# Optimization experiments

Hardware: AMD Instinct MI355X
Metric: run time of the kernel (lower is better)

Reference implementation:

```python
import jax, jax.numpy as jnp
import numpy as np

N_ITERATIONS = 3
N_OUT_CAPS = 10


def squash(t, axis=-2):
    # squash(s) = ||s||^2 * s / ((1 + ||s||^2) * ||s||)
    sqr_norm = jnp.sum(t * t, axis=axis, keepdims=True)
    norm = jnp.sqrt(sqr_norm)
    return sqr_norm * t / ((1.0 + sqr_norm) * norm)


def setup_inputs() -> dict:
    key = jax.random.key(0)
    B, I, O, D = 256, 1152, 10, 16
    u_hat = jax.random.normal(key, (B, I, O, D, 1), dtype=jnp.float32)
    return {"u_hat": u_hat}


def reference(u_hat):
    B = u_hat.shape[0]
    I, O = u_hat.shape[1], u_hat.shape[2]
    # routing logits b: (B, I, O, 1, 1)
    b = jnp.zeros((B, I, O, 1, 1), dtype=u_hat.dtype)
    v = None
    for r in range(N_ITERATIONS):
        c = jax.nn.softmax(b, axis=1)                 # softmax over input capsules
        s = jnp.sum(c * u_hat, axis=1, keepdims=True)  # (B, 1, O, D, 1)
        v = squash(s, axis=-2)
        if r < N_ITERATIONS - 1:
            # u_hat^T @ v: (B,I,O,1,D) @ (B,1,O,D,1) -> (B,I,O,1,1)
            b = b + jnp.matmul(jnp.swapaxes(u_hat, -2, -1), v)
    return v.reshape(B, N_OUT_CAPS, -1)
```

## Files before the change

kernel.cpp:

```cpp
#include <hip/hip_runtime.h>
#include <math.h>

#define N_I 1152
#define N_O 10
#define N_D 16
#define BLK 512
#define KPT 9

__global__ __launch_bounds__(BLK, 4)
void caps_route(const float* __restrict__ u_hat, float* __restrict__ out)
{
    __shared__ float scr_s[8][16];
    __shared__ float scr_e[8];
    __shared__ __align__(16) float vcum[16];

    const int tid  = threadIdx.x;
    const int wave = tid >> 6;
    const int lane = tid & 63;
    const int d4   = tid & 3;
    const int ig   = tid >> 2;

    const int bid = blockIdx.x;
    const int nwg = gridDim.x;
    int wid = bid;
    if ((nwg & 7) == 0) wid = (bid & 7) * (nwg >> 3) + (bid >> 3);
    const int b = wid / N_O;
    const int o = wid - b * N_O;

    const float* gbase = u_hat + (size_t)b * (N_I * N_O * N_D)
                               + (size_t)o * N_D + d4 * 4;

    float4 u[KPT];
    #pragma unroll
    for (int k = 0; k < KPT; ++k) {
        const int i = ig + (k << 7);
        u[k] = *(const float4*)(gbase + (size_t)i * (N_O * N_D));
    }
    if (tid < 16) vcum[tid] = 0.0f;

    float4 vc = make_float4(0.f, 0.f, 0.f, 0.f);

    for (int r = 0; r < 3; ++r) {
        float4 s4 = make_float4(0.f, 0.f, 0.f, 0.f);
        float esum = 0.0f;
        if (r == 0) {
            #pragma unroll
            for (int k = 0; k < KPT; ++k) {
                s4.x += u[k].x; s4.y += u[k].y;
                s4.z += u[k].z; s4.w += u[k].w;
            }
            esum = (float)KPT;
        } else {
            #pragma unroll
            for (int k = 0; k < KPT; ++k) {
                float p = u[k].x*vc.x + u[k].y*vc.y + u[k].z*vc.z + u[k].w*vc.w;
                p += __shfl_xor(p, 1);
                p += __shfl_xor(p, 2);
                const float e = __expf(p);
                esum += e;
                s4.x += e*u[k].x; s4.y += e*u[k].y;
                s4.z += e*u[k].z; s4.w += e*u[k].w;
            }
        }
        #pragma unroll
        for (int m = 4; m <= 32; m <<= 1) {
            s4.x += __shfl_xor(s4.x, m);
            s4.y += __shfl_xor(s4.y, m);
            s4.z += __shfl_xor(s4.z, m);
            s4.w += __shfl_xor(s4.w, m);
            esum += __shfl_xor(esum, m);
        }
        if (lane < 4) {
            scr_s[wave][lane*4+0] = s4.x;
            scr_s[wave][lane*4+1] = s4.y;
            scr_s[wave][lane*4+2] = s4.z;
            scr_s[wave][lane*4+3] = s4.w;
            if (lane == 0) scr_e[wave] = esum;
        }
        __syncthreads();
        if (tid < 16) {
            float s = 0.f, et = 0.f;
            #pragma unroll
            for (int w = 0; w < 8; ++w) { s += scr_s[w][tid]; et += scr_e[w]; }
            s /= et;
            float sq = s * s;
            sq += __shfl_xor(sq, 1);
            sq += __shfl_xor(sq, 2);
            sq += __shfl_xor(sq, 4);
            sq += __shfl_xor(sq, 8);
            const float nrm = sqrtf(sq);
            const float v = s * (nrm / (1.0f + sq));
            if (r == 2) out[(size_t)wid * N_D + tid] = v;
            else        vcum[tid] += v;
        }
        __syncthreads();
        if (r < 2) vc = ((const float4*)vcum)[d4];
    }
}

extern "C" void kernel_launch(void* const* d_in, const int* in_sizes, int n_in,
                              void* d_out, int out_size, void* d_ws, size_t ws_size,
                              hipStream_t stream)
{
    const float* u_hat = (const float*)d_in[0];
    float* out = (float*)d_out;
    const int B = in_sizes[0] / (N_I * N_O * N_D);
    hipLaunchKernelGGL(caps_route, dim3(B * N_O), dim3(BLK), 0, stream, u_hat, out);
}
```

Baseline: 37.03 us.

## Process two output capsules per workgroup to halve block count

Each workgroup now handles a pair of adjacent output capsules, loading two contiguous float4s per input capsule row, and the grid shrinks from B*10 to B*5 blocks. The first-iteration sum is fused into the load loop. This is meant to make each global read cover 128 contiguous bytes instead of 64, and to spread barrier and reduction overhead over twice the work. In exchange, register use doubles (18 float4 held per thread), which may lower occupancy under the launch bounds, and there are fewer blocks to spread across CUs.

```diff
diff --git a/kernel.cpp b/kernel.cpp
--- a/kernel.cpp
+++ b/kernel.cpp
@@ -10,9 +10,9 @@
 __global__ __launch_bounds__(BLK, 4)
 void caps_route(const float* __restrict__ u_hat, float* __restrict__ out)
 {
-    __shared__ float scr_s[8][16];
-    __shared__ float scr_e[8];
-    __shared__ __align__(16) float vcum[16];
+    __shared__ float scr_s[2][8][16];
+    __shared__ float scr_e[2][8];
+    __shared__ __align__(16) float vcum[2][16];
 
     const int tid  = threadIdx.x;
     const int wave = tid >> 6;
@@ -24,64 +24,87 @@
     const int nwg = gridDim.x;
     int wid = bid;
     if ((nwg & 7) == 0) wid = (bid & 7) * (nwg >> 3) + (bid >> 3);
-    const int b = wid / N_O;
-    const int o = wid - b * N_O;
+    const int b  = wid / 5;
+    const int op = wid - b * 5;
+    const int o0 = op * 2;
 
     const float* gbase = u_hat + (size_t)b * (N_I * N_O * N_D)
-                               + (size_t)o * N_D + d4 * 4;
+                               + (size_t)o0 * N_D + d4 * 4;
 
-    float4 u[KPT];
+    float4 u[2][KPT];
+    float4 s4[2];
+    s4[0] = make_float4(0.f, 0.f, 0.f, 0.f);
+    s4[1] = make_float4(0.f, 0.f, 0.f, 0.f);
     #pragma unroll
     for (int k = 0; k < KPT; ++k) {
         const int i = ig + (k << 7);
-        u[k] = *(const float4*)(gbase + (size_t)i * (N_O * N_D));
+        const float* g = gbase + (size_t)i * (N_O * N_D);
+        u[0][k] = *(const float4*)(g);
+        u[1][k] = *(const float4*)(g + N_D);
+        s4[0].x += u[0][k].x; s4[0].y += u[0][k].y;
+        s4[0].z += u[0][k].z; s4[0].w += u[0][k].w;
+        s4[1].x += u[1][k].x; s4[1].y += u[1][k].y;
+        s4[1].z += u[1][k].z; s4[1].w += u[1][k].w;
     }
-    if (tid < 16) vcum[tid] = 0.0f;
+    if (tid < 32) vcum[tid >> 4][tid & 15] = 0.0f;
 
-    float4 vc = make_float4(0.f, 0.f, 0.f, 0.f);
+    float4 vc[2];
+    vc[0] = make_float4(0.f, 0.f, 0.f, 0.f);
+    vc[1] = make_float4(0.f, 0.f, 0.f, 0.f);
 
     for (int r = 0; r < 3; ++r) {
-        float4 s4 = make_float4(0.f, 0.f, 0.f, 0.f);
-        float esum = 0.0f;
+        float esum[2];
         if (r == 0) {
+            esum[0] = (float)KPT; esum[1] = (float)KPT;
+        } else {
+            #pragma unroll
+            for (int j = 0; j < 2; ++j) {
+                s4[j] = make_float4(0.f, 0.f, 0.f, 0.f);
+                esum[j] = 0.0f;
+            }
             #pragma unroll
             for (int k = 0; k < KPT; ++k) {
-                s4.x += u[k].x; s4.y += u[k].y;
-                s4.z += u[k].z; s4.w += u[k].w;
-            }
-            esum = (float)KPT;
-        } else {
-            #pragma unroll
-            for (int k = 0; k < KPT; ++k) {
-                float p = u[k].x*vc.x + u[k].y*vc.y + u[k].z*vc.z + u[k].w*vc.w;
-                p += __shfl_xor(p, 1);
-                p += __shfl_xor(p, 2);
-                const float e = __expf(p);
-                esum += e;
-                s4.x += e*u[k].x; s4.y += e*u[k].y;
-                s4.z += e*u[k].z; s4.w += e*u[k].w;
+                #pragma unroll
+                for (int j = 0; j < 2; ++j) {
+                    float p = u[j][k].x*vc[j].x + u[j][k].y*vc[j].y
+                            + u[j][k].z*vc[j].z + u[j][k].w*vc[j].w;
+                    p += __shfl_xor(p, 1);
+                    p += __shfl_xor(p, 2);
+                    const float e = __expf(p);
+                    esum[j] += e;
+                    s4[j].x += e*u[j][k].x; s4[j].y += e*u[j][k].y;
+                    s4[j].z += e*u[j][k].z; s4[j].w += e*u[j][k].w;
+                }
             }
         }
         #pragma unroll
         for (int m = 4; m <= 32; m <<= 1) {
-            s4.x += __shfl_xor(s4.x, m);
-            s4.y += __shfl_xor(s4.y, m);
-            s4.z += __shfl_xor(s4.z, m);
-            s4.w += __shfl_xor(s4.w, m);
-            esum += __shfl_xor(esum, m);
+            #pragma unroll
+            for (int j = 0; j < 2; ++j) {
+                s4[j].x += __shfl_xor(s4[j].x, m);
+                s4[j].y += __shfl_xor(s4[j].y, m);
+                s4[j].z += __shfl_xor(s4[j].z, m);
+                s4[j].w += __shfl_xor(s4[j].w, m);
+                esum[j] += __shfl_xor(esum[j], m);
+            }
         }
         if (lane < 4) {
-            scr_s[wave][lane*4+0] = s4.x;
-            scr_s[wave][lane*4+1] = s4.y;
-            scr_s[wave][lane*4+2] = s4.z;
-            scr_s[wave][lane*4+3] = s4.w;
-            if (lane == 0) scr_e[wave] = esum;
+            #pragma unroll
+            for (int j = 0; j < 2; ++j) {
+                scr_s[j][wave][lane*4+0] = s4[j].x;
+                scr_s[j][wave][lane*4+1] = s4[j].y;
+                scr_s[j][wave][lane*4+2] = s4[j].z;
+                scr_s[j][wave][lane*4+3] = s4[j].w;
+                if (lane == 0) scr_e[j][wave] = esum[j];
+            }
         }
         __syncthreads();
-        if (tid < 16) {
+        if (tid < 32) {
+            const int j = tid >> 4;
+            const int d = tid & 15;
             float s = 0.f, et = 0.f;
             #pragma unroll
-            for (int w = 0; w < 8; ++w) { s += scr_s[w][tid]; et += scr_e[w]; }
+            for (int w = 0; w < 8; ++w) { s += scr_s[j][w][d]; et += scr_e[j][w]; }
             s /= et;
             float sq = s * s;
             sq += __shfl_xor(sq, 1);
@@ -90,11 +113,14 @@
             sq += __shfl_xor(sq, 8);
             const float nrm = sqrtf(sq);
             const float v = s * (nrm / (1.0f + sq));
-            if (r == 2) out[(size_t)wid * N_D + tid] = v;
-            else        vcum[tid] += v;
+            if (r == 2) out[((size_t)b * N_O + o0 + j) * N_D + d] = v;
+            else        vcum[j][d] += v;
         }
         __syncthreads();
-        if (r < 2) vc = ((const float4*)vcum)[d4];
+        if (r < 2) {
+            vc[0] = ((const float4*)vcum[0])[d4];
+            vc[1] = ((const float4*)vcum[1])[d4];
+        }
     }
 }
 
@@ -105,5 +131,5 @@
     const float* u_hat = (const float*)d_in[0];
     float* out = (float*)d_out;
     const int B = in_sizes[0] / (N_I * N_O * N_D);
-    hipLaunchKernelGGL(caps_route, dim3(B * N_O), dim3(BLK), 0, stream, u_hat, out);
+    hipLaunchKernelGGL(caps_route, dim3(B * 5), dim3(BLK), 0, stream, u_hat, out);
 }
```

New measurement: 39.43 us. 6.5% more time.
